# Optimization experiments

Hardware: AMD Instinct MI355X
Metric: run time of the kernel (lower is better)

Reference implementation:

```python
import jax, jax.numpy as jnp
import numpy as np

N_NODES = 100000
N_EDGES = 1600000
IN_CH = 128
OUT_CH = 64
HID = 2 * OUT_CH  # 128


def setup_inputs() -> dict:
    key = jax.random.key(0)
    ks = jax.random.split(key, 8)
    s = lambda fan_in: 1.0 / np.sqrt(fan_in)
    return {
        "x": jax.random.normal(ks[0], (N_NODES, IN_CH), jnp.float32),
        "edge_index": jax.random.randint(ks[1], (2, N_EDGES), 0, N_NODES, dtype=jnp.int32),
        "W1": jax.random.normal(ks[2], (IN_CH, HID), jnp.float32) * s(IN_CH),
        "b1": jnp.zeros((HID,), jnp.float32),
        "W2": jax.random.normal(ks[3], (HID, HID), jnp.float32) * s(HID),
        "b2": jnp.zeros((HID,), jnp.float32),
        "W3": jax.random.normal(ks[4], (HID, OUT_CH), jnp.float32) * s(HID),
        "b3": jnp.zeros((OUT_CH,), jnp.float32),
    }


def reference(x, edge_index, W1, b1, W2, b2, W3, b3):
    N = x.shape[0]
    # GCNConv (PyG semantics): add self-loops, symmetric deg^{-1/2} normalization,
    # linear transform, scatter-add aggregation at destination, then bias.
    loops = jnp.arange(N, dtype=edge_index.dtype)
    src = jnp.concatenate([edge_index[0], loops])  # [E+N]
    dst = jnp.concatenate([edge_index[1], loops])  # [E+N]
    deg = jnp.zeros((N,), x.dtype).at[dst].add(1.0)  # in-degree incl. self-loop
    dinv = jnp.where(deg > 0, jax.lax.rsqrt(deg), 0.0)
    norm = (dinv[src] * dinv[dst])[:, None]  # [E+N, 1]

    def gcn_conv(h, W, b):
        h = h @ W  # transform first (smaller when out < in)
        msg = h[src] * norm  # gather + normalize, [E+N, C]
        agg = jnp.zeros((N, h.shape[1]), h.dtype).at[dst].add(msg)  # scatter-add
        return agg + b

    h = jax.nn.relu(gcn_conv(x, W1, b1))
    h = jax.nn.relu(gcn_conv(h, W2, b2))
    h = gcn_conv(h, W3, b3)
    return jnp.min(h, axis=0)  # min-pool over nodes -> [OUT_CH]
```

## Files before the change

### kernel.cpp

```cpp
#include <hip/hip_runtime.h>
#include <stdint.h>
#include <stddef.h>
#include <float.h>

typedef short bf16x8 __attribute__((ext_vector_type(8)));
typedef float f32x4 __attribute__((ext_vector_type(4)));

static __device__ __forceinline__ unsigned enc_min(float v) {
  unsigned u = __float_as_uint(v);
  return (u & 0x80000000u) ? ~u : (u | 0x80000000u);
}
static __device__ __forceinline__ unsigned short f2bf(float f) {
  unsigned u = __float_as_uint(f);
  u += 0x7fffu + ((u >> 16) & 1u);
  return (unsigned short)(u >> 16);
}
static __device__ __forceinline__ float bf2f(unsigned short b) {
  return __uint_as_float(((unsigned)b) << 16);
}
static __device__ __forceinline__ void acc8(float* a, uint4 v) {
  a[0] += __uint_as_float(v.x << 16);
  a[1] += __uint_as_float(v.x & 0xffff0000u);
  a[2] += __uint_as_float(v.y << 16);
  a[3] += __uint_as_float(v.y & 0xffff0000u);
  a[4] += __uint_as_float(v.z << 16);
  a[5] += __uint_as_float(v.z & 0xffff0000u);
  a[6] += __uint_as_float(v.w << 16);
  a[7] += __uint_as_float(v.w & 0xffff0000u);
}

__global__ __launch_bounds__(256) void k_count_bin(const int* __restrict__ edge, int E, int N,
                                                   int* __restrict__ cnt8,
                                                   int* __restrict__ bin_cur,
                                                   int2* __restrict__ pairs,
                                                   int binw, int bcap) {
  __shared__ int h[8], gbase[8], lfill[8];
  int cslot = blockIdx.x & 7;
  int* cnt = cnt8 + (size_t)cslot * N;
  int tid = threadIdx.x;
  int nt = (E + 1023) >> 10;
  for (int t = blockIdx.x; t < nt; t += gridDim.x) {
    int e0 = t << 10;
    if (tid < 8) { h[tid] = 0; lfill[tid] = 0; }
    __syncthreads();
    int d[4], s[4], g[4], r[4];
#pragma unroll
    for (int k = 0; k < 4; ++k) {
      int e = e0 + tid + k * 256;
      d[k] = -1;
      if (e < E) {
        d[k] = edge[E + e];
        s[k] = edge[e];
        g[k] = (int)((unsigned)d[k] / (unsigned)binw);
        r[k] = atomicAdd(&cnt[d[k]], 1);
        atomicAdd(&h[g[k]], 1);
      }
    }
    __syncthreads();
    if (tid < 8) gbase[tid] = atomicAdd(&bin_cur[tid], h[tid]);
    __syncthreads();
#pragma unroll
    for (int k = 0; k < 4; ++k) {
      if (d[k] >= 0) {
        int rr = atomicAdd(&lfill[g[k]], 1);
        int p = gbase[g[k]] + rr;
        unsigned packed = (unsigned)d[k] | ((unsigned)cslot << 17) | ((unsigned)r[k] << 20);
        if (p < bcap) pairs[(size_t)g[k] * bcap + p] = make_int2((int)packed, s[k]);
      }
    }
    __syncthreads();
  }
}

__global__ void k_scan1(const int* __restrict__ cnt8, int N,
                        int* __restrict__ cnt, int* __restrict__ incl,
                        int* __restrict__ bsum) {
  __shared__ int sm[1024];
  int tid = threadIdx.x;
  int i = blockIdx.x * 1024 + tid;
  int v = 0;
  if (i < N) {
#pragma unroll
    for (int g = 0; g < 8; ++g) v += cnt8[(size_t)g * N + i];
    cnt[i] = v;
  }
  sm[tid] = v;
  __syncthreads();
  for (int off = 1; off < 1024; off <<= 1) {
    int t = (tid >= off) ? sm[tid - off] : 0;
    __syncthreads();
    sm[tid] += t;
    __syncthreads();
  }
  if (i < N) incl[i] = sm[tid];
  if (tid == 1023) bsum[blockIdx.x] = sm[1023];
}

__global__ void k_scan2(const int* __restrict__ bsum, int nb, int* __restrict__ boff) {
  __shared__ int sm[128];
  int tid = threadIdx.x;
  int v = (tid < nb) ? bsum[tid] : 0;
  sm[tid] = v;
  __syncthreads();
  for (int off = 1; off < 128; off <<= 1) {
    int t = (tid >= off) ? sm[tid - off] : 0;
    __syncthreads();
    sm[tid] += t;
    __syncthreads();
  }
  if (tid < nb) boff[tid] = sm[tid] - v;
}

__global__ void k_aux(const int* __restrict__ cnt, const int* __restrict__ cnt8,
                      const int* __restrict__ incl, const int* __restrict__ boff,
                      int N, int E, int* __restrict__ row_ptr,
                      int* __restrict__ base8, float* __restrict__ dinv) {
  int i = blockIdx.x * blockDim.x + threadIdx.x;
  if (i < N) {
    int rp = incl[i] - cnt[i] + boff[i >> 10];
    row_ptr[i] = rp;
    dinv[i] = 1.0f / sqrtf((float)(cnt[i] + 1));
    int run = rp;
#pragma unroll
    for (int c = 0; c < 8; ++c) {
      base8[(size_t)c * N + i] = run;
      run += cnt8[(size_t)c * N + i];
    }
  } else if (i == N) {
    row_ptr[N] = E;
  }
}

__global__ void k_prepw(const float* __restrict__ W1, const float* __restrict__ W2,
                        const float* __restrict__ W3,
                        unsigned short* __restrict__ w1h, unsigned short* __restrict__ w1l,
                        unsigned short* __restrict__ w2h, unsigned short* __restrict__ w2l,
                        unsigned short* __restrict__ w3h, unsigned short* __restrict__ w3l) {
  const int K = 128;
  int idx = blockIdx.x * 256 + threadIdx.x;
  const float* W;
  unsigned short *oh, *ol;
  int Nn, base;
  if (idx < 16384) { W = W1; Nn = 128; oh = w1h; ol = w1l; base = idx; }
  else if (idx < 32768) { W = W2; Nn = 128; oh = w2h; ol = w2l; base = idx - 16384; }
  else if (idx < 40960) { W = W3; Nn = 64; oh = w3h; ol = w3l; base = idx - 32768; }
  else return;
  int n = base / K, k = base % K;
  float w = W[(size_t)k * Nn + n];
  unsigned short h = f2bf(w);
  unsigned short l = f2bf(w - bf2f(h));
  int nf = n >> 4, mloc = n & 15, kci = k >> 5, quad = (k >> 3) & 3, j = k & 7;
  size_t o = ((size_t)((nf * 4 + kci) * 64 + quad * 16 + mloc)) * 8 + j;
  oh[o] = h;
  ol[o] = l;
}

template <int NFW>
static __device__ __forceinline__ void gemm_body(const float* __restrict__ A,
                                                 const unsigned short* __restrict__ Wfh,
                                                 const unsigned short* __restrict__ Wfl,
                                                 const float* __restrict__ dinv,
                                                 unsigned short* __restrict__ P, int M,
                                                 int blk) {
  const int K = 128;
  const int COUT = NFW * 64;
  __shared__ unsigned short Ah[64][136];
  __shared__ unsigned short Al[64][136];
  int tid = threadIdx.x;
  int m0 = blk * 64;
  int w = tid >> 6, lane = tid & 63;

  bf16x8 bh[NFW][4], bl[NFW][4];
#pragma unroll
  for (int i = 0; i < NFW; ++i)
#pragma unroll
    for (int kci = 0; kci < 4; ++kci) {
      size_t o = ((size_t)(((w * NFW + i) * 4 + kci) * 64 + lane)) * 8;
      bh[i][kci] = *(const bf16x8*)&Wfh[o];
      bl[i][kci] = *(const bf16x8*)&Wfl[o];
    }

#pragma unroll
  for (int q = 0; q < 8; ++q) {
    int f = q * 256 + tid;
    int m = f >> 5, k4 = f & 31;
    int row = m0 + m;
    if (row >= M) row = M - 1;
    float4 v = *(const float4*)&A[(size_t)row * K + k4 * 4];
    unsigned short h0 = f2bf(v.x), h1 = f2bf(v.y), h2 = f2bf(v.z), h3 = f2bf(v.w);
    unsigned short l0 = f2bf(v.x - bf2f(h0)), l1 = f2bf(v.y - bf2f(h1));
    unsigned short l2 = f2bf(v.z - bf2f(h2)), l3 = f2bf(v.w - bf2f(h3));
    uint2 hh, ll;
    hh.x = (unsigned)h0 | ((unsigned)h1 << 16);
    hh.y = (unsigned)h2 | ((unsigned)h3 << 16);
    ll.x = (unsigned)l0 | ((unsigned)l1 << 16);
    ll.y = (unsigned)l2 | ((unsigned)l3 << 16);
    *(uint2*)&Ah[m][k4 * 4] = hh;
    *(uint2*)&Al[m][k4 * 4] = ll;
  }
  __syncthreads();

  int mloc = lane & 15, quad = lane >> 4;
  f32x4 acc[4][NFW];
#pragma unroll
  for (int rt = 0; rt < 4; ++rt)
#pragma unroll
    for (int i = 0; i < NFW; ++i) acc[rt][i] = (f32x4){0.f, 0.f, 0.f, 0.f};

#pragma unroll
  for (int rt = 0; rt < 4; ++rt) {
    const unsigned short* ph = &Ah[rt * 16 + mloc][quad * 8];
    const unsigned short* pl = &Al[rt * 16 + mloc][quad * 8];
#pragma unroll
    for (int kci = 0; kci < 4; ++kci) {
      bf16x8 ah = *(const bf16x8*)(ph + kci * 32);
      bf16x8 al = *(const bf16x8*)(pl + kci * 32);
#pragma unroll
      for (int i = 0; i < NFW; ++i) {
        acc[rt][i] = __builtin_amdgcn_mfma_f32_16x16x32_bf16(al, bh[i][kci], acc[rt][i], 0, 0, 0);
        acc[rt][i] = __builtin_amdgcn_mfma_f32_16x16x32_bf16(ah, bl[i][kci], acc[rt][i], 0, 0, 0);
        acc[rt][i] = __builtin_amdgcn_mfma_f32_16x16x32_bf16(ah, bh[i][kci], acc[rt][i], 0, 0, 0);
      }
    }
  }

#pragma unroll
  for (int rt = 0; rt < 4; ++rt) {
    int rbase = m0 + rt * 16 + quad * 4;
#pragma unroll
    for (int r = 0; r < 4; ++r) {
      int row = rbase + r;
      if (row < M) {
        float dv = dinv[row];
#pragma unroll
        for (int i = 0; i < NFW; ++i) {
          int nf = w * NFW + i;
          P[(size_t)row * COUT + nf * 16 + mloc] = f2bf(acc[rt][i][r] * dv);
        }
      }
    }
  }
}

__global__ __launch_bounds__(256) void k_fill_gemm(const float* __restrict__ A,
                                                   const unsigned short* __restrict__ Wfh,
                                                   const unsigned short* __restrict__ Wfl,
                                                   const float* __restrict__ dinv,
                                                   unsigned short* __restrict__ P, int M,
                                                   const int2* __restrict__ pairs,
                                                   const int* __restrict__ bin_cur, int bcap,
                                                   const int* __restrict__ base8, int N,
                                                   int* __restrict__ srcs, int ns) {
  if ((int)blockIdx.x >= ns) {
    gemm_body<2>(A, Wfh, Wfl, dinv, P, M, blockIdx.x - ns);
  } else {
    int grp = blockIdx.x & 7;
    int bslot = blockIdx.x >> 3;
    int nslot = ns >> 3;
    int cnt_g = bin_cur[grp];
    if (cnt_g > bcap) cnt_g = bcap;
    const int2* pp = pairs + (size_t)grp * bcap;
    for (int i = bslot * blockDim.x + threadIdx.x; i < cnt_g; i += nslot * blockDim.x) {
      int2 pr = pp[i];
      unsigned w = (unsigned)pr.x;
      int d = (int)(w & 0x1FFFFu);
      int c = (int)((w >> 17) & 7u);
      int r = (int)(w >> 20);
      srcs[base8[(size_t)c * N + d] + r] = pr.y;
    }
  }
}

template <int NFW>
__global__ __launch_bounds__(256) void k_agg_gemm(const unsigned short* __restrict__ Pin,
                                                  const int* __restrict__ row_ptr,
                                                  const int* __restrict__ srcs,
                                                  const float* __restrict__ dinv,
                                                  const float* __restrict__ bias,
                                                  const unsigned short* __restrict__ Wfh,
                                                  const unsigned short* __restrict__ Wfl,
                                                  unsigned short* __restrict__ Pout, int N) {
  const int COUT = NFW * 64;
  __shared__ unsigned short Ah[16][136];
  __shared__ unsigned short Al[16][136];
  int tid = threadIdx.x;
  int wv = tid >> 6, lane = tid & 63;
  int grp = lane >> 4, sub = lane & 15;
  int m = wv * 4 + grp;
  int d = blockIdx.x * 16 + m;
  int dc = d < N ? d : N - 1;
  bool valid = d < N;
  unsigned soff = (unsigned)sub * 16u;
  const char* Pb = (const char*)Pin;

  float a[8] = {0.f, 0.f, 0.f, 0.f, 0.f, 0.f, 0.f, 0.f};
  {
    uint4 v = *(const uint4*)(Pb + ((unsigned)dc * 256u + soff));
    acc8(a, v);
  }
  int lo = row_ptr[dc];
  int hi = row_ptr[valid ? d + 1 : dc];
  int j = lo;
  for (; j + 4 <= hi; j += 4) {
    unsigned i0 = (unsigned)srcs[j];
    unsigned i1 = (unsigned)srcs[j + 1];
    unsigned i2 = (unsigned)srcs[j + 2];
    unsigned i3 = (unsigned)srcs[j + 3];
    uint4 v0 = *(const uint4*)(Pb + (i0 * 256u + soff));
    uint4 v1 = *(const uint4*)(Pb + (i1 * 256u + soff));
    uint4 v2 = *(const uint4*)(Pb + (i2 * 256u + soff));
    uint4 v3 = *(const uint4*)(Pb + (i3 * 256u + soff));
    acc8(a, v0);
    acc8(a, v1);
    acc8(a, v2);
    acc8(a, v3);
  }
  for (; j < hi; ++j) {
    unsigned i0 = (unsigned)srcs[j];
    uint4 v0 = *(const uint4*)(Pb + (i0 * 256u + soff));
    acc8(a, v0);
  }

  bf16x8 bh[NFW][4], bl[NFW][4];
#pragma unroll
  for (int i = 0; i < NFW; ++i)
#pragma unroll
    for (int kci = 0; kci < 4; ++kci) {
      size_t o = ((size_t)(((wv * NFW + i) * 4 + kci) * 64 + lane)) * 8;
      bh[i][kci] = *(const bf16x8*)&Wfh[o];
      bl[i][kci] = *(const bf16x8*)&Wfl[o];
    }

  float dv = dinv[dc];
  int ch0 = sub * 8;
  float4 bv0 = *(const float4*)&bias[ch0];
  float4 bv1 = *(const float4*)&bias[ch0 + 4];
  float h[8];
  h[0] = dv * a[0] + bv0.x; h[1] = dv * a[1] + bv0.y;
  h[2] = dv * a[2] + bv0.z; h[3] = dv * a[3] + bv0.w;
  h[4] = dv * a[4] + bv1.x; h[5] = dv * a[5] + bv1.y;
  h[6] = dv * a[6] + bv1.z; h[7] = dv * a[7] + bv1.w;
#pragma unroll
  for (int k = 0; k < 8; ++k) h[k] = fmaxf(h[k], 0.f);
  unsigned short hb[8], lb[8];
#pragma unroll
  for (int k = 0; k < 8; ++k) {
    hb[k] = f2bf(h[k]);
    lb[k] = f2bf(h[k] - bf2f(hb[k]));
  }
  uint4 HH, LL;
  HH.x = (unsigned)hb[0] | ((unsigned)hb[1] << 16);
  HH.y = (unsigned)hb[2] | ((unsigned)hb[3] << 16);
  HH.z = (unsigned)hb[4] | ((unsigned)hb[5] << 16);
  HH.w = (unsigned)hb[6] | ((unsigned)hb[7] << 16);
  LL.x = (unsigned)lb[0] | ((unsigned)lb[1] << 16);
  LL.y = (unsigned)lb[2] | ((unsigned)lb[3] << 16);
  LL.z = (unsigned)lb[4] | ((unsigned)lb[5] << 16);
  LL.w = (unsigned)lb[6] | ((unsigned)lb[7] << 16);
  *(uint4*)&Ah[m][ch0] = HH;
  *(uint4*)&Al[m][ch0] = LL;
  __syncthreads();

  int mloc = lane & 15, quad = lane >> 4;
  f32x4 acc[NFW];
#pragma unroll
  for (int i = 0; i < NFW; ++i) acc[i] = (f32x4){0.f, 0.f, 0.f, 0.f};
#pragma unroll
  for (int kci = 0; kci < 4; ++kci) {
    bf16x8 ah = *(const bf16x8*)&Ah[mloc][quad * 8 + kci * 32];
    bf16x8 al = *(const bf16x8*)&Al[mloc][quad * 8 + kci * 32];
#pragma unroll
    for (int i = 0; i < NFW; ++i) {
      acc[i] = __builtin_amdgcn_mfma_f32_16x16x32_bf16(al, bh[i][kci], acc[i], 0, 0, 0);
      acc[i] = __builtin_amdgcn_mfma_f32_16x16x32_bf16(ah, bl[i][kci], acc[i], 0, 0, 0);
      acc[i] = __builtin_amdgcn_mfma_f32_16x16x32_bf16(ah, bh[i][kci], acc[i], 0, 0, 0);
    }
  }
  int rbase = blockIdx.x * 16 + quad * 4;
#pragma unroll
  for (int r = 0; r < 4; ++r) {
    int row = rbase + r;
    if (row < N) {
      float dvr = dinv[row];
#pragma unroll
      for (int i = 0; i < NFW; ++i) {
        int nf = wv * NFW + i;
        Pout[(size_t)row * COUT + nf * 16 + mloc] = f2bf(acc[i][r] * dvr);
      }
    }
  }
}

__global__ __launch_bounds__(256) void k_agg_pool(const unsigned short* __restrict__ P,
                                                  const int* __restrict__ row_ptr,
                                                  const int* __restrict__ srcs,
                                                  const float* __restrict__ dinv,
                                                  const float* __restrict__ bias,
                                                  unsigned* __restrict__ minenc, int N) {
  const int CAP = 448;
  __shared__ int s_idx[4][CAP];
  __shared__ float s_red[4][32];
  int tid = threadIdx.x;
  int wv = tid >> 6, lane = tid & 63;
  int b8 = blockIdx.x & 7;
  int slice = b8 >> 2, part = b8 & 3;
  int g0 = ((blockIdx.x >> 3) * 4 + part) * 64 + wv * 16;
  const char* Pb = (const char*)P + slice * 64;

  int i = lane >> 2, q = lane & 3;
  unsigned qoff = (unsigned)q * 16u;
  int d = g0 + i;
  int dc = d < N ? d : N - 1;
  bool valid = d < N;

  int e0 = row_ptr[g0 < N ? g0 : N];
  int e1 = row_ptr[(g0 + 16) < N ? (g0 + 16) : N];
  int lo_n = row_ptr[dc];
  int hi_n = row_ptr[valid ? d + 1 : dc];

  float a[8];
  {
    uint4 v = *(const uint4*)(Pb + ((unsigned)dc * 128u + qoff));
    a[0] = __uint_as_float(v.x << 16);
    a[1] = __uint_as_float(v.x & 0xffff0000u);
    a[2] = __uint_as_float(v.y << 16);
    a[3] = __uint_as_float(v.y & 0xffff0000u);
    a[4] = __uint_as_float(v.z << 16);
    a[5] = __uint_as_float(v.z & 0xffff0000u);
    a[6] = __uint_as_float(v.w << 16);
    a[7] = __uint_as_float(v.w & 0xffff0000u);
  }

  for (int w0 = e0; w0 < e1; w0 += CAP) {
    int wend = min(w0 + CAP, e1);
    int cnt = wend - w0;
    __builtin_amdgcn_wave_barrier();
    for (int t = lane; t < cnt; t += 64) s_idx[wv][t] = srcs[w0 + t];
    __builtin_amdgcn_wave_barrier();
    int j = max(lo_n, w0), hi = min(hi_n, wend);
    for (; j + 4 <= hi; j += 4) {
      unsigned i0 = (unsigned)s_idx[wv][j - w0];
      unsigned i1 = (unsigned)s_idx[wv][j - w0 + 1];
      unsigned i2 = (unsigned)s_idx[wv][j - w0 + 2];
      unsigned i3 = (unsigned)s_idx[wv][j - w0 + 3];
      uint4 v0 = *(const uint4*)(Pb + (i0 * 128u + qoff));
      uint4 v1 = *(const uint4*)(Pb + (i1 * 128u + qoff));
      uint4 v2 = *(const uint4*)(Pb + (i2 * 128u + qoff));
      uint4 v3 = *(const uint4*)(Pb + (i3 * 128u + qoff));
      acc8(a, v0);
      acc8(a, v1);
      acc8(a, v2);
      acc8(a, v3);
    }
    for (; j < hi; ++j) {
      unsigned i0 = (unsigned)s_idx[wv][j - w0];
      uint4 v0 = *(const uint4*)(Pb + (i0 * 128u + qoff));
      acc8(a, v0);
    }
  }

  int c0 = slice * 32 + q * 8;
  float dv = dinv[dc];
  float4 bv0 = *(const float4*)&bias[c0];
  float4 bv1 = *(const float4*)&bias[c0 + 4];
  float h[8];
  h[0] = dv * a[0] + bv0.x; h[1] = dv * a[1] + bv0.y;
  h[2] = dv * a[2] + bv0.z; h[3] = dv * a[3] + bv0.w;
  h[4] = dv * a[4] + bv1.x; h[5] = dv * a[5] + bv1.y;
  h[6] = dv * a[6] + bv1.z; h[7] = dv * a[7] + bv1.w;

  if (!valid) {
#pragma unroll
    for (int k = 0; k < 8; ++k) h[k] = FLT_MAX;
  }
#pragma unroll
  for (int off = 4; off < 64; off <<= 1) {
#pragma unroll
    for (int k = 0; k < 8; ++k) h[k] = fminf(h[k], __shfl_xor(h[k], off, 64));
  }
  if (lane < 4) {
#pragma unroll
    for (int k = 0; k < 8; ++k) s_red[wv][q * 8 + k] = h[k];
  }
  __syncthreads();
  if (tid < 32) {
    float mn = fminf(fminf(s_red[0][tid], s_red[1][tid]),
                     fminf(s_red[2][tid], s_red[3][tid]));
    atomicMin(&minenc[slice * 32 + tid], enc_min(mn));
  }
}

__global__ void k_decode(const unsigned* __restrict__ minenc, float* __restrict__ out) {
  int c = threadIdx.x;
  unsigned k = minenc[c];
  unsigned u = (k & 0x80000000u) ? (k & 0x7FFFFFFFu) : ~k;
  out[c] = __uint_as_float(u);
}

extern "C" void kernel_launch(void* const* d_in, const int* in_sizes, int n_in,
                              void* d_out, int out_size, void* d_ws, size_t ws_size,
                              hipStream_t stream) {
  const float* X  = (const float*)d_in[0];
  const int* edge = (const int*)d_in[1];
  const float* W1 = (const float*)d_in[2];
  const float* b1 = (const float*)d_in[3];
  const float* W2 = (const float*)d_in[4];
  const float* b2 = (const float*)d_in[5];
  const float* W3 = (const float*)d_in[6];
  const float* b3 = (const float*)d_in[7];
  float* out = (float*)d_out;

  const int IN_CH = 128;
  int N = in_sizes[0] / IN_CH;
  int E = in_sizes[1] / 2;

  char* ws = (char*)d_ws;
  size_t off = 0;
  auto alloc = [&](size_t bytes) {
    void* p = ws + off;
    off = (off + bytes + 255) & ~(size_t)255;
    return p;
  };
  unsigned short* P1 = (unsigned short*)alloc((size_t)N * 128 * 2);
  unsigned short* P2 = (unsigned short*)alloc((size_t)N * 128 * 2);
  int* srcs      = (int*)alloc((size_t)E * 4);
  int* cnt8      = (int*)alloc((size_t)8 * N * 4);
  int* base8     = (int*)alloc((size_t)8 * N * 4);
  int* cnt       = (int*)alloc((size_t)N * 4);
  int* incl      = (int*)alloc((size_t)N * 4);
  int* row_ptr   = (int*)alloc((size_t)(N + 1) * 4);
  float* dinv    = (float*)alloc((size_t)N * 4);
  int* bsum      = (int*)alloc(1024);
  int* boff      = (int*)alloc(1024);
  int* bin_cur   = (int*)alloc(256);
  unsigned* minenc = (unsigned*)alloc(256);
  unsigned short* w1h = (unsigned short*)alloc(16384 * 2);
  unsigned short* w1l = (unsigned short*)alloc(16384 * 2);
  unsigned short* w2h = (unsigned short*)alloc(16384 * 2);
  unsigned short* w2l = (unsigned short*)alloc(16384 * 2);
  unsigned short* w3h = (unsigned short*)alloc(8192 * 2);
  unsigned short* w3l = (unsigned short*)alloc(8192 * 2);

  int bcap = E / 8 + 65536;
  int binw = (N + 7) / 8;
  int2* pairs = (int2*)P2;
  unsigned short* P3 = P1;

  hipMemsetAsync(cnt8, 0, (size_t)8 * N * 4, stream);
  hipMemsetAsync(bin_cur, 0, 32, stream);
  hipMemsetAsync(minenc, 0xFF, 64 * 4, stream);

  int nb = (N + 1023) / 1024;
  int gx = (N + 63) / 64;
  int ns = 1024;
  int gagg = (N + 15) / 16;
  int c64 = (N + 255) / 256;
  k_prepw<<<160, 256, 0, stream>>>(W1, W2, W3, w1h, w1l, w2h, w2l, w3h, w3l);
  k_count_bin<<<782, 256, 0, stream>>>(edge, E, N, cnt8, bin_cur, pairs, binw, bcap);
  k_scan1<<<nb, 1024, 0, stream>>>(cnt8, N, cnt, incl, bsum);
  k_scan2<<<1, 128, 0, stream>>>(bsum, nb, boff);
  k_aux<<<(N + 256) / 256, 256, 0, stream>>>(cnt, cnt8, incl, boff, N, E, row_ptr, base8, dinv);

  k_fill_gemm<<<ns + gx, 256, 0, stream>>>(X, w1h, w1l, dinv, P1, N,
                                           pairs, bin_cur, bcap, base8, N, srcs, ns);
  k_agg_gemm<2><<<gagg, 256, 0, stream>>>(P1, row_ptr, srcs, dinv, b1, w2h, w2l, P2, N);
  k_agg_gemm<1><<<gagg, 256, 0, stream>>>(P2, row_ptr, srcs, dinv, b2, w3h, w3l, P3, N);
  k_agg_pool<<<c64 * 8, 256, 0, stream>>>(P3, row_ptr, srcs, dinv, b3, minenc, N);
  k_decode<<<1, 64, 0, stream>>>(minenc, out);
}
```

Baseline: 420.6 us.

## Overlap first GEMM with edge counting and apply source normalization in aggregation

The first-layer GEMM no longer scales its output by dinv, so it can run in the same launch as the edge count/bin kernel instead of waiting for the degree scan. The CSR scatter becomes its own kernel. Aggregation loops now load dinv[src] per edge and use FMA weighting, with an 8-wide unrolled gather. The pooling kernel is restructured to one node per 8 lanes covering all 64 channels, dropping the shared-memory index staging. The cost is an extra dinv gather per edge and one more kernel launch.

```diff
diff --git a/kernel.cpp b/kernel.cpp
--- a/kernel.cpp
+++ b/kernel.cpp
@@ -18,117 +18,15 @@
 static __device__ __forceinline__ float bf2f(unsigned short b) {
   return __uint_as_float(((unsigned)b) << 16);
 }
-static __device__ __forceinline__ void acc8(float* a, uint4 v) {
-  a[0] += __uint_as_float(v.x << 16);
-  a[1] += __uint_as_float(v.x & 0xffff0000u);
-  a[2] += __uint_as_float(v.y << 16);
-  a[3] += __uint_as_float(v.y & 0xffff0000u);
-  a[4] += __uint_as_float(v.z << 16);
-  a[5] += __uint_as_float(v.z & 0xffff0000u);
-  a[6] += __uint_as_float(v.w << 16);
-  a[7] += __uint_as_float(v.w & 0xffff0000u);
-}
-
-__global__ __launch_bounds__(256) void k_count_bin(const int* __restrict__ edge, int E, int N,
-                                                   int* __restrict__ cnt8,
-                                                   int* __restrict__ bin_cur,
-                                                   int2* __restrict__ pairs,
-                                                   int binw, int bcap) {
-  __shared__ int h[8], gbase[8], lfill[8];
-  int cslot = blockIdx.x & 7;
-  int* cnt = cnt8 + (size_t)cslot * N;
-  int tid = threadIdx.x;
-  int nt = (E + 1023) >> 10;
-  for (int t = blockIdx.x; t < nt; t += gridDim.x) {
-    int e0 = t << 10;
-    if (tid < 8) { h[tid] = 0; lfill[tid] = 0; }
-    __syncthreads();
-    int d[4], s[4], g[4], r[4];
-#pragma unroll
-    for (int k = 0; k < 4; ++k) {
-      int e = e0 + tid + k * 256;
-      d[k] = -1;
-      if (e < E) {
-        d[k] = edge[E + e];
-        s[k] = edge[e];
-        g[k] = (int)((unsigned)d[k] / (unsigned)binw);
-        r[k] = atomicAdd(&cnt[d[k]], 1);
-        atomicAdd(&h[g[k]], 1);
-      }
-    }
-    __syncthreads();
-    if (tid < 8) gbase[tid] = atomicAdd(&bin_cur[tid], h[tid]);
-    __syncthreads();
-#pragma unroll
-    for (int k = 0; k < 4; ++k) {
-      if (d[k] >= 0) {
-        int rr = atomicAdd(&lfill[g[k]], 1);
-        int p = gbase[g[k]] + rr;
-        unsigned packed = (unsigned)d[k] | ((unsigned)cslot << 17) | ((unsigned)r[k] << 20);
-        if (p < bcap) pairs[(size_t)g[k] * bcap + p] = make_int2((int)packed, s[k]);
-      }
-    }
-    __syncthreads();
-  }
-}
-
-__global__ void k_scan1(const int* __restrict__ cnt8, int N,
-                        int* __restrict__ cnt, int* __restrict__ incl,
-                        int* __restrict__ bsum) {
-  __shared__ int sm[1024];
-  int tid = threadIdx.x;
-  int i = blockIdx.x * 1024 + tid;
-  int v = 0;
-  if (i < N) {
-#pragma unroll
-    for (int g = 0; g < 8; ++g) v += cnt8[(size_t)g * N + i];
-    cnt[i] = v;
-  }
-  sm[tid] = v;
-  __syncthreads();
-  for (int off = 1; off < 1024; off <<= 1) {
-    int t = (tid >= off) ? sm[tid - off] : 0;
-    __syncthreads();
-    sm[tid] += t;
-    __syncthreads();
-  }
-  if (i < N) incl[i] = sm[tid];
-  if (tid == 1023) bsum[blockIdx.x] = sm[1023];
-}
-
-__global__ void k_scan2(const int* __restrict__ bsum, int nb, int* __restrict__ boff) {
-  __shared__ int sm[128];
-  int tid = threadIdx.x;
-  int v = (tid < nb) ? bsum[tid] : 0;
-  sm[tid] = v;
-  __syncthreads();
-  for (int off = 1; off < 128; off <<= 1) {
-    int t = (tid >= off) ? sm[tid - off] : 0;
-    __syncthreads();
-    sm[tid] += t;
-    __syncthreads();
-  }
-  if (tid < nb) boff[tid] = sm[tid] - v;
-}
-
-__global__ void k_aux(const int* __restrict__ cnt, const int* __restrict__ cnt8,
-                      const int* __restrict__ incl, const int* __restrict__ boff,
-                      int N, int E, int* __restrict__ row_ptr,
-                      int* __restrict__ base8, float* __restrict__ dinv) {
-  int i = blockIdx.x * blockDim.x + threadIdx.x;
-  if (i < N) {
-    int rp = incl[i] - cnt[i] + boff[i >> 10];
-    row_ptr[i] = rp;
-    dinv[i] = 1.0f / sqrtf((float)(cnt[i] + 1));
-    int run = rp;
-#pragma unroll
-    for (int c = 0; c < 8; ++c) {
-      base8[(size_t)c * N + i] = run;
-      run += cnt8[(size_t)c * N + i];
-    }
-  } else if (i == N) {
-    row_ptr[N] = E;
-  }
+static __device__ __forceinline__ void acc8w(float* a, uint4 v, float w) {
+  a[0] = fmaf(w, __uint_as_float(v.x << 16), a[0]);
+  a[1] = fmaf(w, __uint_as_float(v.x & 0xffff0000u), a[1]);
+  a[2] = fmaf(w, __uint_as_float(v.y << 16), a[2]);
+  a[3] = fmaf(w, __uint_as_float(v.y & 0xffff0000u), a[3]);
+  a[4] = fmaf(w, __uint_as_float(v.z << 16), a[4]);
+  a[5] = fmaf(w, __uint_as_float(v.z & 0xffff0000u), a[5]);
+  a[6] = fmaf(w, __uint_as_float(v.w << 16), a[6]);
+  a[7] = fmaf(w, __uint_as_float(v.w & 0xffff0000u), a[7]);
 }
 
 __global__ void k_prepw(const float* __restrict__ W1, const float* __restrict__ W2,
@@ -159,7 +57,6 @@
 static __device__ __forceinline__ void gemm_body(const float* __restrict__ A,
                                                  const unsigned short* __restrict__ Wfh,
                                                  const unsigned short* __restrict__ Wfl,
-                                                 const float* __restrict__ dinv,
                                                  unsigned short* __restrict__ P, int M,
                                                  int blk) {
   const int K = 128;
@@ -231,43 +128,144 @@
     for (int r = 0; r < 4; ++r) {
       int row = rbase + r;
       if (row < M) {
-        float dv = dinv[row];
 #pragma unroll
         for (int i = 0; i < NFW; ++i) {
           int nf = w * NFW + i;
-          P[(size_t)row * COUT + nf * 16 + mloc] = f2bf(acc[rt][i][r] * dv);
+          P[(size_t)row * COUT + nf * 16 + mloc] = f2bf(acc[rt][i][r]);
         }
       }
     }
   }
 }
 
-__global__ __launch_bounds__(256) void k_fill_gemm(const float* __restrict__ A,
-                                                   const unsigned short* __restrict__ Wfh,
-                                                   const unsigned short* __restrict__ Wfl,
-                                                   const float* __restrict__ dinv,
-                                                   unsigned short* __restrict__ P, int M,
-                                                   const int2* __restrict__ pairs,
-                                                   const int* __restrict__ bin_cur, int bcap,
-                                                   const int* __restrict__ base8, int N,
-                                                   int* __restrict__ srcs, int ns) {
-  if ((int)blockIdx.x >= ns) {
-    gemm_body<2>(A, Wfh, Wfl, dinv, P, M, blockIdx.x - ns);
-  } else {
-    int grp = blockIdx.x & 7;
-    int bslot = blockIdx.x >> 3;
-    int nslot = ns >> 3;
-    int cnt_g = bin_cur[grp];
-    if (cnt_g > bcap) cnt_g = bcap;
-    const int2* pp = pairs + (size_t)grp * bcap;
-    for (int i = bslot * blockDim.x + threadIdx.x; i < cnt_g; i += nslot * blockDim.x) {
-      int2 pr = pp[i];
-      unsigned w = (unsigned)pr.x;
-      int d = (int)(w & 0x1FFFFu);
-      int c = (int)((w >> 17) & 7u);
-      int r = (int)(w >> 20);
-      srcs[base8[(size_t)c * N + d] + r] = pr.y;
-    }
+__global__ __launch_bounds__(256) void k_count_gemm(const int* __restrict__ edge, int E, int N,
+                                                    int* __restrict__ cnt8,
+                                                    int* __restrict__ bin_cur,
+                                                    int2* __restrict__ pairs,
+                                                    int binw, int bcap,
+                                                    const float* __restrict__ X,
+                                                    const unsigned short* __restrict__ w1h,
+                                                    const unsigned short* __restrict__ w1l,
+                                                    unsigned short* __restrict__ P1,
+                                                    int ncb) {
+  if ((int)blockIdx.x >= ncb) {
+    gemm_body<2>(X, w1h, w1l, P1, N, blockIdx.x - ncb);
+    return;
+  }
+  __shared__ int h[8], gbase[8], lfill[8];
+  int cslot = blockIdx.x & 7;
+  int* cnt = cnt8 + (size_t)cslot * N;
+  int tid = threadIdx.x;
+  int nt = (E + 1023) >> 10;
+  for (int t = blockIdx.x; t < nt; t += ncb) {
+    int e0 = t << 10;
+    if (tid < 8) { h[tid] = 0; lfill[tid] = 0; }
+    __syncthreads();
+    int d[4], s[4], g[4], r[4];
+#pragma unroll
+    for (int k = 0; k < 4; ++k) {
+      int e = e0 + tid + k * 256;
+      d[k] = -1;
+      if (e < E) {
+        d[k] = edge[E + e];
+        s[k] = edge[e];
+        g[k] = (int)((unsigned)d[k] / (unsigned)binw);
+        r[k] = atomicAdd(&cnt[d[k]], 1);
+        atomicAdd(&h[g[k]], 1);
+      }
+    }
+    __syncthreads();
+    if (tid < 8) gbase[tid] = atomicAdd(&bin_cur[tid], h[tid]);
+    __syncthreads();
+#pragma unroll
+    for (int k = 0; k < 4; ++k) {
+      if (d[k] >= 0) {
+        int rr = atomicAdd(&lfill[g[k]], 1);
+        int p = gbase[g[k]] + rr;
+        unsigned packed = (unsigned)d[k] | ((unsigned)cslot << 17) | ((unsigned)r[k] << 20);
+        if (p < bcap) pairs[(size_t)g[k] * bcap + p] = make_int2((int)packed, s[k]);
+      }
+    }
+    __syncthreads();
+  }
+}
+
+__global__ void k_scan1(const int* __restrict__ cnt8, int N,
+                        int* __restrict__ cnt, int* __restrict__ incl,
+                        int* __restrict__ bsum) {
+  __shared__ int sm[1024];
+  int tid = threadIdx.x;
+  int i = blockIdx.x * 1024 + tid;
+  int v = 0;
+  if (i < N) {
+#pragma unroll
+    for (int g = 0; g < 8; ++g) v += cnt8[(size_t)g * N + i];
+    cnt[i] = v;
+  }
+  sm[tid] = v;
+  __syncthreads();
+  for (int off = 1; off < 1024; off <<= 1) {
+    int t = (tid >= off) ? sm[tid - off] : 0;
+    __syncthreads();
+    sm[tid] += t;
+    __syncthreads();
+  }
+  if (i < N) incl[i] = sm[tid];
+  if (tid == 1023) bsum[blockIdx.x] = sm[1023];
+}
+
+__global__ void k_scan2(const int* __restrict__ bsum, int nb, int* __restrict__ boff) {
+  __shared__ int sm[128];
+  int tid = threadIdx.x;
+  int v = (tid < nb) ? bsum[tid] : 0;
+  sm[tid] = v;
+  __syncthreads();
+  for (int off = 1; off < 128; off <<= 1) {
+    int t = (tid >= off) ? sm[tid - off] : 0;
+    __syncthreads();
+    sm[tid] += t;
+    __syncthreads();
+  }
+  if (tid < nb) boff[tid] = sm[tid] - v;
+}
+
+__global__ void k_aux(const int* __restrict__ cnt, const int* __restrict__ cnt8,
+                      const int* __restrict__ incl, const int* __restrict__ boff,
+                      int N, int E, int* __restrict__ row_ptr,
+                      int* __restrict__ base8, float* __restrict__ dinv) {
+  int i = blockIdx.x * blockDim.x + threadIdx.x;
+  if (i < N) {
+    int rp = incl[i] - cnt[i] + boff[i >> 10];
+    row_ptr[i] = rp;
+    dinv[i] = 1.0f / sqrtf((float)(cnt[i] + 1));
+    int run = rp;
+#pragma unroll
+    for (int c = 0; c < 8; ++c) {
+      base8[(size_t)c * N + i] = run;
+      run += cnt8[(size_t)c * N + i];
+    }
+  } else if (i == N) {
+    row_ptr[N] = E;
+  }
+}
+
+__global__ __launch_bounds__(256) void k_scatter(const int2* __restrict__ pairs,
+                                                 const int* __restrict__ bin_cur, int bcap,
+                                                 const int* __restrict__ base8, int N,
+                                                 int* __restrict__ srcs) {
+  int grp = blockIdx.x & 7;
+  int bslot = blockIdx.x >> 3;
+  int nslot = gridDim.x >> 3;
+  int cnt_g = bin_cur[grp];
+  if (cnt_g > bcap) cnt_g = bcap;
+  const int2* pp = pairs + (size_t)grp * bcap;
+  for (int i = bslot * blockDim.x + threadIdx.x; i < cnt_g; i += nslot * blockDim.x) {
+    int2 pr = pp[i];
+    unsigned w = (unsigned)pr.x;
+    int d = (int)(w & 0x1FFFFu);
+    int c = (int)((w >> 17) & 7u);
+    int r = (int)(w >> 20);
+    srcs[base8[(size_t)c * N + d] + r] = pr.y;
   }
 }
 
@@ -293,32 +291,46 @@
   unsigned soff = (unsigned)sub * 16u;
   const char* Pb = (const char*)Pin;
 
+  float dv = dinv[dc];
   float a[8] = {0.f, 0.f, 0.f, 0.f, 0.f, 0.f, 0.f, 0.f};
   {
     uint4 v = *(const uint4*)(Pb + ((unsigned)dc * 256u + soff));
-    acc8(a, v);
+    acc8w(a, v, dv);
   }
   int lo = row_ptr[dc];
   int hi = row_ptr[valid ? d + 1 : dc];
   int j = lo;
+  for (; j + 8 <= hi; j += 8) {
+    unsigned id[8];
+    float dw[8];
+    uint4 vv[8];
+#pragma unroll
+    for (int k = 0; k < 8; ++k) id[k] = (unsigned)srcs[j + k];
+#pragma unroll
+    for (int k = 0; k < 8; ++k) dw[k] = dinv[id[k]];
+#pragma unroll
+    for (int k = 0; k < 8; ++k) vv[k] = *(const uint4*)(Pb + (id[k] * 256u + soff));
+#pragma unroll
+    for (int k = 0; k < 8; ++k) acc8w(a, vv[k], dw[k]);
+  }
   for (; j + 4 <= hi; j += 4) {
-    unsigned i0 = (unsigned)srcs[j];
-    unsigned i1 = (unsigned)srcs[j + 1];
-    unsigned i2 = (unsigned)srcs[j + 2];
-    unsigned i3 = (unsigned)srcs[j + 3];
-    uint4 v0 = *(const uint4*)(Pb + (i0 * 256u + soff));
-    uint4 v1 = *(const uint4*)(Pb + (i1 * 256u + soff));
-    uint4 v2 = *(const uint4*)(Pb + (i2 * 256u + soff));
-    uint4 v3 = *(const uint4*)(Pb + (i3 * 256u + soff));
-    acc8(a, v0);
-    acc8(a, v1);
-    acc8(a, v2);
-    acc8(a, v3);
+    unsigned id[4];
+    float dw[4];
+    uint4 vv[4];
+#pragma unroll
+    for (int k = 0; k < 4; ++k) id[k] = (unsigned)srcs[j + k];
+#pragma unroll
+    for (int k = 0; k < 4; ++k) dw[k] = dinv[id[k]];
+#pragma unroll
+    for (int k = 0; k < 4; ++k) vv[k] = *(const uint4*)(Pb + (id[k] * 256u + soff));
+#pragma unroll
+    for (int k = 0; k < 4; ++k) acc8w(a, vv[k], dw[k]);
   }
   for (; j < hi; ++j) {
     unsigned i0 = (unsigned)srcs[j];
+    float w0 = dinv[i0];
     uint4 v0 = *(const uint4*)(Pb + (i0 * 256u + soff));
-    acc8(a, v0);
+    acc8w(a, v0, w0);
   }
 
   bf16x8 bh[NFW][4], bl[NFW][4];
@@ -331,7 +343,6 @@
       bl[i][kci] = *(const bf16x8*)&Wfl[o];
     }
 
-  float dv = dinv[dc];
   int ch0 = sub * 8;
   float4 bv0 = *(const float4*)&bias[ch0];
   float4 bv1 = *(const float4*)&bias[ch0 + 4];
@@ -381,11 +392,10 @@
   for (int r = 0; r < 4; ++r) {
     int row = rbase + r;
     if (row < N) {
-      float dvr = dinv[row];
 #pragma unroll
       for (int i = 0; i < NFW; ++i) {
         int nf = wv * NFW + i;
-        Pout[(size_t)row * COUT + nf * 16 + mloc] = f2bf(acc[i][r] * dvr);
+        Pout[(size_t)row * COUT + nf * 16 + mloc] = f2bf(acc[i][r]);
       }
     }
   }
@@ -397,70 +407,46 @@
                                                   const float* __restrict__ dinv,
                                                   const float* __restrict__ bias,
                                                   unsigned* __restrict__ minenc, int N) {
-  const int CAP = 448;
-  __shared__ int s_idx[4][CAP];
-  __shared__ float s_red[4][32];
+  __shared__ float s_red[4][64];
   int tid = threadIdx.x;
   int wv = tid >> 6, lane = tid & 63;
-  int b8 = blockIdx.x & 7;
-  int slice = b8 >> 2, part = b8 & 3;
-  int g0 = ((blockIdx.x >> 3) * 4 + part) * 64 + wv * 16;
-  const char* Pb = (const char*)P + slice * 64;
-
-  int i = lane >> 2, q = lane & 3;
-  unsigned qoff = (unsigned)q * 16u;
-  int d = g0 + i;
-  int dc = d < N ? d : N - 1;
+  int g = lane >> 3, q = lane & 7;
+  int d = blockIdx.x * 32 + wv * 8 + g;
   bool valid = d < N;
-
-  int e0 = row_ptr[g0 < N ? g0 : N];
-  int e1 = row_ptr[(g0 + 16) < N ? (g0 + 16) : N];
-  int lo_n = row_ptr[dc];
-  int hi_n = row_ptr[valid ? d + 1 : dc];
-
-  float a[8];
+  int dc = valid ? d : N - 1;
+  const char* Pb = (const char*)P;
+  unsigned soff = (unsigned)q * 16u;
+
+  float dv = dinv[dc];
+  float a[8] = {0.f, 0.f, 0.f, 0.f, 0.f, 0.f, 0.f, 0.f};
   {
-    uint4 v = *(const uint4*)(Pb + ((unsigned)dc * 128u + qoff));
-    a[0] = __uint_as_float(v.x << 16);
-    a[1] = __uint_as_float(v.x & 0xffff0000u);
-    a[2] = __uint_as_float(v.y << 16);
-    a[3] = __uint_as_float(v.y & 0xffff0000u);
-    a[4] = __uint_as_float(v.z << 16);
-    a[5] = __uint_as_float(v.z & 0xffff0000u);
-    a[6] = __uint_as_float(v.w << 16);
-    a[7] = __uint_as_float(v.w & 0xffff0000u);
-  }
-
-  for (int w0 = e0; w0 < e1; w0 += CAP) {
-    int wend = min(w0 + CAP, e1);
-    int cnt = wend - w0;
-    __builtin_amdgcn_wave_barrier();
-    for (int t = lane; t < cnt; t += 64) s_idx[wv][t] = srcs[w0 + t];
-    __builtin_amdgcn_wave_barrier();
-    int j = max(lo_n, w0), hi = min(hi_n, wend);
-    for (; j + 4 <= hi; j += 4) {
-      unsigned i0 = (unsigned)s_idx[wv][j - w0];
-      unsigned i1 = (unsigned)s_idx[wv][j - w0 + 1];
-      unsigned i2 = (unsigned)s_idx[wv][j - w0 + 2];
-      unsigned i3 = (unsigned)s_idx[wv][j - w0 + 3];
-      uint4 v0 = *(const uint4*)(Pb + (i0 * 128u + qoff));
-      uint4 v1 = *(const uint4*)(Pb + (i1 * 128u + qoff));
-      uint4 v2 = *(const uint4*)(Pb + (i2 * 128u + qoff));
-      uint4 v3 = *(const uint4*)(Pb + (i3 * 128u + qoff));
-      acc8(a, v0);
-      acc8(a, v1);
-      acc8(a, v2);
-      acc8(a, v3);
-    }
-    for (; j < hi; ++j) {
-      unsigned i0 = (unsigned)s_idx[wv][j - w0];
-      uint4 v0 = *(const uint4*)(Pb + (i0 * 128u + qoff));
-      acc8(a, v0);
-    }
-  }
-
-  int c0 = slice * 32 + q * 8;
-  float dv = dinv[dc];
+    uint4 v = *(const uint4*)(Pb + ((unsigned)dc * 128u + soff));
+    acc8w(a, v, dv);
+  }
+  int lo = row_ptr[dc];
+  int hi = row_ptr[valid ? d + 1 : dc];
+  int j = lo;
+  for (; j + 8 <= hi; j += 8) {
+    unsigned id[8];
+    float dw[8];
+    uint4 vv[8];
+#pragma unroll
+    for (int k = 0; k < 8; ++k) id[k] = (unsigned)srcs[j + k];
+#pragma unroll
+    for (int k = 0; k < 8; ++k) dw[k] = dinv[id[k]];
+#pragma unroll
+    for (int k = 0; k < 8; ++k) vv[k] = *(const uint4*)(Pb + (id[k] * 128u + soff));
+#pragma unroll
+    for (int k = 0; k < 8; ++k) acc8w(a, vv[k], dw[k]);
+  }
+  for (; j < hi; ++j) {
+    unsigned i0 = (unsigned)srcs[j];
+    float w0 = dinv[i0];
+    uint4 v0 = *(const uint4*)(Pb + (i0 * 128u + soff));
+    acc8w(a, v0, w0);
+  }
+
+  int c0 = q * 8;
   float4 bv0 = *(const float4*)&bias[c0];
   float4 bv1 = *(const float4*)&bias[c0 + 4];
   float h[8];
@@ -468,25 +454,24 @@
   h[2] = dv * a[2] + bv0.z; h[3] = dv * a[3] + bv0.w;
   h[4] = dv * a[4] + bv1.x; h[5] = dv * a[5] + bv1.y;
   h[6] = dv * a[6] + bv1.z; h[7] = dv * a[7] + bv1.w;
-
   if (!valid) {
 #pragma unroll
     for (int k = 0; k < 8; ++k) h[k] = FLT_MAX;
   }
 #pragma unroll
-  for (int off = 4; off < 64; off <<= 1) {
+  for (int off = 8; off < 64; off <<= 1) {
 #pragma unroll
     for (int k = 0; k < 8; ++k) h[k] = fminf(h[k], __shfl_xor(h[k], off, 64));
   }
-  if (lane < 4) {
+  if (lane < 8) {
 #pragma unroll
     for (int k = 0; k < 8; ++k) s_red[wv][q * 8 + k] = h[k];
   }
   __syncthreads();
-  if (tid < 32) {
+  if (tid < 64) {
     float mn = fminf(fminf(s_red[0][tid], s_red[1][tid]),
                      fminf(s_red[2][tid], s_red[3][tid]));
-    atomicMin(&minenc[slice * 32 + tid], enc_min(mn));
+    atomicMin(&minenc[tid], enc_min(mn));
   }
 }
 
@@ -552,19 +537,18 @@
 
   int nb = (N + 1023) / 1024;
   int gx = (N + 63) / 64;
-  int ns = 1024;
+  int ncb = 782;
   int gagg = (N + 15) / 16;
-  int c64 = (N + 255) / 256;
+  int gpool = (N + 31) / 32;
   k_prepw<<<160, 256, 0, stream>>>(W1, W2, W3, w1h, w1l, w2h, w2l, w3h, w3l);
-  k_count_bin<<<782, 256, 0, stream>>>(edge, E, N, cnt8, bin_cur, pairs, binw, bcap);
+  k_count_gemm<<<ncb + gx, 256, 0, stream>>>(edge, E, N, cnt8, bin_cur, pairs, binw, bcap,
+                                             X, w1h, w1l, P1, ncb);
   k_scan1<<<nb, 1024, 0, stream>>>(cnt8, N, cnt, incl, bsum);
   k_scan2<<<1, 128, 0, stream>>>(bsum, nb, boff);
   k_aux<<<(N + 256) / 256, 256, 0, stream>>>(cnt, cnt8, incl, boff, N, E, row_ptr, base8, dinv);
-
-  k_fill_gemm<<<ns + gx, 256, 0, stream>>>(X, w1h, w1l, dinv, P1, N,
-                                           pairs, bin_cur, bcap, base8, N, srcs, ns);
+  k_scatter<<<2048, 256, 0, stream>>>(pairs, bin_cur, bcap, base8, N, srcs);
   k_agg_gemm<2><<<gagg, 256, 0, stream>>>(P1, row_ptr, srcs, dinv, b1, w2h, w2l, P2, N);
   k_agg_gemm<1><<<gagg, 256, 0, stream>>>(P2, row_ptr, srcs, dinv, b2, w3h, w3l, P3, N);
-  k_agg_pool<<<c64 * 8, 256, 0, stream>>>(P3, row_ptr, srcs, dinv, b3, minenc, N);
+  k_agg_pool<<<gpool, 256, 0, stream>>>(P3, row_ptr, srcs, dinv, b3, minenc, N);
   k_decode<<<1, 64, 0, stream>>>(minenc, out);
 }
```

Result: slower. 436.9 us (+3.9%).
